# Performance work log

Hardware: AMD Instinct MI355X
Metric: run time of the kernel (lower is better)

## Reference

```python
import jax, jax.numpy as jnp
import numpy as np


def setup_inputs() -> dict:
    key = jax.random.key(0)
    k1, k2, k3 = jax.random.split(key, 3)
    bs, seqlen, hidden = 2, 2048, 1024
    s, h = 4, 256  # sqrt_n_heads, head_size
    std = 0.02
    num_layers = 12
    hidden_states = jax.random.normal(k1, (bs, seqlen, hidden), dtype=jnp.float32)
    q_scale = 1.0 / np.sqrt(2.0 * num_layers * h)
    queries = jax.random.normal(k2, (s, h, h * s), dtype=jnp.float32) * std * q_scale
    combiners = jax.random.normal(k3, (s, h * s, h), dtype=jnp.float32) * (std * q_scale)
    return {"hidden_states": hidden_states, "queries": queries, "combiners": combiners}


def reference(hidden_states, queries, combiners):
    # queries: [s1, h, s*h], combiners: [s1, s*h, h]
    s, h, _ = queries.shape
    bs, S, E = hidden_states.shape
    x = hidden_states.reshape(bs, S, s, h)            # [b, t, s, h]
    qw = queries.reshape(s, h, s, h)                  # [s1, h_in, s2, h_out]
    # projected queries, already permuted to [s2, b, t, s1, f]
    Q = jnp.einsum('btae,aeqf->qbtaf', x, qw)
    # pre-attention scores: [s2, b, t, s1, u] (u = key position)  ~O(S^2)
    pre = jnp.einsum('qbtaf,buqf->qbtau', Q, x)
    # attention output, permuted to [s1, b, t, s2, g]
    attn = jnp.einsum('qbtau,buqg->abtqg', pre, x)
    attn = attn.reshape(s, bs, S, s * h)              # [s1, b, t, s2*h]
    out = jnp.einsum('abtk,akg->btag', attn, combiners)
    return out.reshape(bs, S, s * h)
```

## Files before the change

kernel.cpp:

```cpp
#include <hip/hip_runtime.h>
#include <hip/hip_bf16.h>


typedef unsigned short u16;
using short8  = __attribute__((ext_vector_type(8))) short;
using floatx4 = __attribute__((ext_vector_type(4))) float;

__device__ inline u16 f2bf(float f) {
    unsigned u = __float_as_uint(f);
    unsigned r = u + 0x7fffu + ((u >> 16) & 1u);
    return (u16)(r >> 16);
}

template <typename T>
__device__ inline void stage64(const T* __restrict__ src, long ld,
                               u16* __restrict__ dst, int tid) {
#pragma unroll
    for (int it = 0; it < 4; ++it) {
        const int flat = (it * 256 + tid) * 4;
        const int kl = flat & 63, rl = flat >> 6;
        ushort4 v;
        if (sizeof(T) == 4) {
            const float4 f = *(const float4*)&((const float*)src)[(long)rl * ld + kl];
            v.x = f2bf(f.x); v.y = f2bf(f.y); v.z = f2bf(f.z); v.w = f2bf(f.w);
        } else {
            v = *(const ushort4*)&((const u16*)src)[(long)rl * ld + kl];
        }
        const int chunk = ((kl >> 5) * 4 + (rl >> 4)) * 64 + ((kl >> 3) & 3) * 16 + (rl & 15);
        *(ushort4*)&dst[chunk * 8 + (kl & 7)] = v;
    }
}

__device__ inline void stage64_sum8(const float* __restrict__ s0, long ld,
                                    long partStride,
                                    u16* __restrict__ dst, int tid) {
#pragma unroll
    for (int it = 0; it < 4; ++it) {
        const int flat = (it * 256 + tid) * 4;
        const int kl = flat & 63, rl = flat >> 6;
        const long off = (long)rl * ld + kl;
        float4 acc = *(const float4*)&s0[off];
#pragma unroll
        for (int s = 1; s < 8; ++s) {
            const float4 f = *(const float4*)&s0[(long)s * partStride + off];
            acc.x += f.x; acc.y += f.y; acc.z += f.z; acc.w += f.w;
        }
        ushort4 v;
        v.x = f2bf(acc.x); v.y = f2bf(acc.y); v.z = f2bf(acc.z); v.w = f2bf(acc.w);
        const int chunk = ((kl >> 5) * 4 + (rl >> 4)) * 64 + ((kl >> 3) & 3) * 16 + (rl & 15);
        *(ushort4*)&dst[chunk * 8 + (kl & 7)] = v;
    }
}

__device__ inline void stage_km64(const float* __restrict__ src, long ld,
                                  u16* __restrict__ dst, int tid) {
#pragma unroll
    for (int it = 0; it < 4; ++it) {
        const int flat = (it * 256 + tid) * 4;
        const int m = flat & 63, k = flat >> 6;
        const float4 f = *(const float4*)&src[(long)k * ld + m];
        const int cb_ = ((k >> 5) * 4 + (m >> 4)) * 64 + ((k & 31) >> 3) * 16 + (m & 15);
        const int j = k & 7;
        dst[(cb_ + 0) * 8 + j] = f2bf(f.x);
        dst[(cb_ + 1) * 8 + j] = f2bf(f.y);
        dst[(cb_ + 2) * 8 + j] = f2bf(f.z);
        dst[(cb_ + 3) * 8 + j] = f2bf(f.w);
    }
}

template <typename TA, typename TB, typename TC,
          bool AKM, bool BKM, bool BSUM8, bool ATOMIC>
__device__ inline void gemm_tile(const TA* __restrict__ A, long lda,
                                 const TB* __restrict__ B, long ldb,
                                 long partStride,
                                 TC* __restrict__ C, long ldc,
                                 int m0, int n0) {
    __shared__ u16 As[16384];
    __shared__ u16 Bs[16384];
    const int tid = threadIdx.x, lane = tid & 63, w = tid >> 6;
    const int IA = (w & 1) * 2, JB = (w >> 1) * 2;
    floatx4 acc[2][2] = {};

#pragma unroll
    for (int kb = 0; kb < 4; ++kb) {
        if (AKM) stage_km64((const float*)A + (long)(kb * 64) * lda, lda, As + kb * 4096, tid);
        else     stage64(A + kb * 64, lda, As + kb * 4096, tid);
    }
#pragma unroll
    for (int kb = 0; kb < 4; ++kb) {
        if (BSUM8)    stage64_sum8((const float*)B + kb * 64, ldb, partStride, Bs + kb * 4096, tid);
        else if (BKM) stage_km64((const float*)B + (long)(kb * 64) * ldb, ldb, Bs + kb * 4096, tid);
        else          stage64(B + kb * 64, ldb, Bs + kb * 4096, tid);
    }
    __syncthreads();

#pragma unroll
    for (int kb = 0; kb < 4; ++kb)
#pragma unroll
        for (int s = 0; s < 2; ++s) {
            short8 af[2], bfr[2];
#pragma unroll
            for (int i = 0; i < 2; ++i)
                af[i] = *(const short8*)&As[kb * 4096 + ((s * 4 + IA + i) * 64 + lane) * 8];
#pragma unroll
            for (int j = 0; j < 2; ++j)
                bfr[j] = *(const short8*)&Bs[kb * 4096 + ((s * 4 + JB + j) * 64 + lane) * 8];
#pragma unroll
            for (int i = 0; i < 2; ++i)
#pragma unroll
                for (int j = 0; j < 2; ++j)
                    acc[i][j] = __builtin_amdgcn_mfma_f32_16x16x32_bf16(af[i], bfr[j], acc[i][j], 0, 0, 0);
        }

    const int rb = (lane >> 4) * 4, col = lane & 15;
#pragma unroll
    for (int i = 0; i < 2; ++i)
#pragma unroll
        for (int j = 0; j < 2; ++j)
#pragma unroll
            for (int r = 0; r < 4; ++r) {
                const int gm = m0 + (IA + i) * 16 + rb + r;
                const int gn = n0 + (JB + j) * 16 + col;
                TC* p = &C[(long)gm * ldc + gn];
                if (sizeof(TC) == 2) *(u16*)p = f2bf(acc[i][j][r]);
                else if (ATOMIC) atomicAdd((float*)p, acc[i][j][r]);
                else *(float*)p = acc[i][j][r];
            }
}

__global__ __launch_bounds__(256) void k_cvt(const float* __restrict__ x,
                                             u16* __restrict__ xbf) {
    const long i = ((long)blockIdx.x * 256 + threadIdx.x) * 8;
    const float4 a = *(const float4*)&x[i];
    const float4 b = *(const float4*)&x[i + 4];
    ushort4 lo, hi;
    lo.x = f2bf(a.x); lo.y = f2bf(a.y); lo.z = f2bf(a.z); lo.w = f2bf(a.w);
    hi.x = f2bf(b.x); hi.y = f2bf(b.y); hi.z = f2bf(b.z); hi.w = f2bf(b.w);
    *(ushort4*)&xbf[i]     = lo;
    *(ushort4*)&xbf[i + 4] = hi;
}

__global__ __launch_bounds__(256) void k_gred(const float* __restrict__ Gp,
                                              float* __restrict__ Gs) {
    const long i = ((long)blockIdx.x * 256 + threadIdx.x) * 4;
    float4 acc = *(const float4*)&Gp[i];
#pragma unroll
    for (int s = 1; s < 8; ++s) {
        const float4 f = *(const float4*)&Gp[(long)s * 524288 + i];
        acc.x += f.x; acc.y += f.y; acc.z += f.z; acc.w += f.w;
    }
    *(float4*)&Gs[i] = acc;
}

__device__ inline void stage_km128_bf(const u16* __restrict__ src, long ld,
                                      u16* __restrict__ dst, int tid) {
#pragma unroll
    for (int it = 0; it < 4; ++it) {
        const int flat = (it * 256 + tid) * 8;
        const int m = flat & 127, k = flat >> 7;
        const short8 v = *(const short8*)&src[(long)k * ld + m];
        const int cb_ = ((k >> 5) * 8 + (m >> 4)) * 64 + ((k & 31) >> 3) * 16 + (m & 15);
        const int j = k & 7;
#pragma unroll
        for (int e = 0; e < 8; ++e)
            dst[(cb_ + e) * 8 + j] = (u16)v[e];
    }
}

__global__ __launch_bounds__(256) void k_gram(const u16* __restrict__ xbf,
                                              float* __restrict__ Gp,
                                              float* __restrict__ Wt) {
    __shared__ u16 As[16384];
    __shared__ u16 Bs[16384];
    const int tl = blockIdx.x, bq = blockIdx.y, split = blockIdx.z;
    const int tm = tl >> 1, tn = tl & 1;
    const int b = bq >> 2, q = bq & 3;
    const int tid = threadIdx.x, lane = tid & 63, w = tid >> 6;
    const int IA2 = (w & 1), JB2 = (w >> 1);

    {
        const int bl = tl + 4 * bq + 32 * split;
        float4 zero = {0.f, 0.f, 0.f, 0.f};
        float4* wz = (float4*)(Wt + (long)bl * 2048) + tid;
        wz[0] = zero; wz[256] = zero;
    }

    const u16* base = xbf + (long)b * 2097152 + (long)split * 256 * 1024 + q * 256;
    const u16* A = base + tm * 128;
    const u16* B = base + tn * 128;
    floatx4 acc[4][4] = {};

#pragma unroll
    for (int burst = 0; burst < 2; ++burst) {
        if (burst) __syncthreads();
#pragma unroll
        for (int kb = 0; kb < 2; ++kb) {
            const long kk = burst * 128 + kb * 64;
            stage_km128_bf(A + kk * 1024, 1024, As + kb * 8192, tid);
            stage_km128_bf(B + kk * 1024, 1024, Bs + kb * 8192, tid);
        }
        __syncthreads();
#pragma unroll
        for (int kb = 0; kb < 2; ++kb)
#pragma unroll
            for (int s = 0; s < 2; ++s) {
                short8 af[4], bfr[4];
#pragma unroll
                for (int i = 0; i < 4; ++i)
                    af[i] = *(const short8*)&As[kb * 8192 + ((s * 8 + IA2 * 4 + i) * 64 + lane) * 8];
#pragma unroll
                for (int j = 0; j < 4; ++j)
                    bfr[j] = *(const short8*)&Bs[kb * 8192 + ((s * 8 + JB2 * 4 + j) * 64 + lane) * 8];
#pragma unroll
                for (int i = 0; i < 4; ++i)
#pragma unroll
                    for (int j = 0; j < 4; ++j)
                        acc[i][j] = __builtin_amdgcn_mfma_f32_16x16x32_bf16(af[i], bfr[j], acc[i][j], 0, 0, 0);
            }
    }

    float* C = Gp + (long)(split * 8 + bq) * 65536;
    const int rb = (lane >> 4) * 4, col = lane & 15;
#pragma unroll
    for (int i = 0; i < 4; ++i)
#pragma unroll
        for (int j = 0; j < 4; ++j)
#pragma unroll
            for (int r = 0; r < 4; ++r) {
                const int gm = tm * 128 + IA2 * 64 + i * 16 + rb + r;
                const int gn = tn * 128 + JB2 * 64 + j * 16 + col;
                C[(long)gm * 256 + gn] = acc[i][j][r];
            }
}

__global__ __launch_bounds__(256) void k_2a(const float* __restrict__ comb,
                                            const float* __restrict__ Gs,
                                            u16* __restrict__ Tt) {
    const int tile = blockIdx.x, i = blockIdx.y;
    const int tm = tile >> 2, tn = tile & 3;
    const int q = i & 3, ba = i >> 2, b = ba >> 2, a = ba & 3;
    gemm_tile<float, float, u16, true, false, false, false>(
        comb + (long)a * 262144 + (long)q * 256 * 256 + tm * 64, 256,
        Gs + (long)(b * 4 + q) * 65536 + (long)tn * 64 * 256, 256,
        0,
        Tt + (long)ba * 262144, 1024,
        tm * 64, q * 256 + tn * 64);
}

__global__ __launch_bounds__(256) void k_2b(const u16* __restrict__ Tt,
                                            const float* __restrict__ qw,
                                            float* __restrict__ Wt) {
    const int tile = blockIdx.x, ba = blockIdx.y, split = blockIdx.z;
    const int tm = tile >> 2, tn = tile & 3;
    const int a = ba & 3;
    gemm_tile<u16, float, float, false, false, false, true>(
        Tt + (long)ba * 262144 + (long)tm * 64 * 1024 + split * 256, 1024,
        qw + (long)a * 262144 + (long)tn * 64 * 1024 + split * 256, 1024, 0,
        Wt + (long)ba * 65536, 256,
        tm * 64, tn * 64);
}

__global__ __launch_bounds__(256) void k_3(const u16* __restrict__ xbf,
                                           const float* __restrict__ Wt,
                                           float* __restrict__ out) {
    const int tl = blockIdx.x, ba = blockIdx.y;
    const int tm = tl >> 2, tn = tl & 3;
    const int b = ba >> 2, a = ba & 3;
    gemm_tile<u16, float, float, false, false, false, false>(
        xbf + (long)b * 2097152 + (long)tm * 64 * 1024 + a * 256, 1024,
        Wt + (long)ba * 65536 + (long)tn * 64 * 256, 256, 0,
        out + (long)b * 2097152 + a * 256, 1024,
        tm * 64, tn * 64);
}

extern "C" void kernel_launch(void* const* d_in, const int* in_sizes, int n_in,
                              void* d_out, int out_size, void* d_ws, size_t ws_size,
                              hipStream_t stream) {
    const float* x    = (const float*)d_in[0];
    const float* qw   = (const float*)d_in[1];
    const float* comb = (const float*)d_in[2];
    float* out = (float*)d_out;

    char* ws = (char*)d_ws;
    float* Gp = (float*)(ws);
    float* Wt = (float*)(ws + (16u << 20));
    u16*   Tt = (u16*)  (ws + (18u << 20));
    float* Gs = (float*)(ws + (22u << 20));
    u16*   xbf= (u16*)  (ws + (24u << 20));

    k_cvt <<<dim3(2048),     256, 0, stream>>>(x, xbf);
    k_gram<<<dim3(4, 8, 8),  256, 0, stream>>>(xbf, Gp, Wt);
    k_gred<<<dim3(512),      256, 0, stream>>>(Gp, Gs);
    k_2a  <<<dim3(16, 32),   256, 0, stream>>>(comb, Gs, Tt);
    k_2b  <<<dim3(16, 8, 4), 256, 0, stream>>>(Tt, qw, Wt);
    k_3   <<<dim3(128, 8),   256, 0, stream>>>(xbf, Wt, out);
}
```

Before: 133.7 us.

## Pre-convert weights to bf16, drop atomics in k_2b, store intermediates as bf16

A single prep kernel now converts x, queries, and a transposed combiners tensor to bf16 up front. All GEMM stages then stage only bf16 operands with 16-byte loads. k_2b loops over the full K with four rounds instead of a 4-way split with atomicAdd, which also removes the Wt zeroing. Gs and Wt are stored as bf16, halving their traffic. The cost is an extra transpose pass, fewer blocks in k_2b (128 instead of 512), and slightly more rounding in the intermediates.

```diff
diff --git a/kernel.cpp b/kernel.cpp
--- a/kernel.cpp
+++ b/kernel.cpp
@@ -12,69 +12,23 @@
     return (u16)(r >> 16);
 }
 
-template <typename T>
-__device__ inline void stage64(const T* __restrict__ src, long ld,
-                               u16* __restrict__ dst, int tid) {
-#pragma unroll
-    for (int it = 0; it < 4; ++it) {
-        const int flat = (it * 256 + tid) * 4;
+__device__ inline void stage64_bf(const u16* __restrict__ src, long ld,
+                                  u16* __restrict__ dst, int tid) {
+#pragma unroll
+    for (int it = 0; it < 2; ++it) {
+        const int flat = (it * 256 + tid) * 8;
         const int kl = flat & 63, rl = flat >> 6;
-        ushort4 v;
-        if (sizeof(T) == 4) {
-            const float4 f = *(const float4*)&((const float*)src)[(long)rl * ld + kl];
-            v.x = f2bf(f.x); v.y = f2bf(f.y); v.z = f2bf(f.z); v.w = f2bf(f.w);
-        } else {
-            v = *(const ushort4*)&((const u16*)src)[(long)rl * ld + kl];
-        }
+        const short8 v = *(const short8*)&src[(long)rl * ld + kl];
         const int chunk = ((kl >> 5) * 4 + (rl >> 4)) * 64 + ((kl >> 3) & 3) * 16 + (rl & 15);
-        *(ushort4*)&dst[chunk * 8 + (kl & 7)] = v;
-    }
-}
-
-__device__ inline void stage64_sum8(const float* __restrict__ s0, long ld,
-                                    long partStride,
-                                    u16* __restrict__ dst, int tid) {
-#pragma unroll
-    for (int it = 0; it < 4; ++it) {
-        const int flat = (it * 256 + tid) * 4;
-        const int kl = flat & 63, rl = flat >> 6;
-        const long off = (long)rl * ld + kl;
-        float4 acc = *(const float4*)&s0[off];
-#pragma unroll
-        for (int s = 1; s < 8; ++s) {
-            const float4 f = *(const float4*)&s0[(long)s * partStride + off];
-            acc.x += f.x; acc.y += f.y; acc.z += f.z; acc.w += f.w;
-        }
-        ushort4 v;
-        v.x = f2bf(acc.x); v.y = f2bf(acc.y); v.z = f2bf(acc.z); v.w = f2bf(acc.w);
-        const int chunk = ((kl >> 5) * 4 + (rl >> 4)) * 64 + ((kl >> 3) & 3) * 16 + (rl & 15);
-        *(ushort4*)&dst[chunk * 8 + (kl & 7)] = v;
-    }
-}
-
-__device__ inline void stage_km64(const float* __restrict__ src, long ld,
-                                  u16* __restrict__ dst, int tid) {
-#pragma unroll
-    for (int it = 0; it < 4; ++it) {
-        const int flat = (it * 256 + tid) * 4;
-        const int m = flat & 63, k = flat >> 6;
-        const float4 f = *(const float4*)&src[(long)k * ld + m];
-        const int cb_ = ((k >> 5) * 4 + (m >> 4)) * 64 + ((k & 31) >> 3) * 16 + (m & 15);
-        const int j = k & 7;
-        dst[(cb_ + 0) * 8 + j] = f2bf(f.x);
-        dst[(cb_ + 1) * 8 + j] = f2bf(f.y);
-        dst[(cb_ + 2) * 8 + j] = f2bf(f.z);
-        dst[(cb_ + 3) * 8 + j] = f2bf(f.w);
-    }
-}
-
-template <typename TA, typename TB, typename TC,
-          bool AKM, bool BKM, bool BSUM8, bool ATOMIC>
-__device__ inline void gemm_tile(const TA* __restrict__ A, long lda,
-                                 const TB* __restrict__ B, long ldb,
-                                 long partStride,
-                                 TC* __restrict__ C, long ldc,
-                                 int m0, int n0) {
+        *(short8*)&dst[chunk * 8] = v;
+    }
+}
+
+template <typename TC, int KR>
+__device__ inline void gemm64(const u16* __restrict__ A, long lda,
+                              const u16* __restrict__ B, long ldb,
+                              TC* __restrict__ C, long ldc,
+                              int m0, int n0) {
     __shared__ u16 As[16384];
     __shared__ u16 Bs[16384];
     const int tid = threadIdx.x, lane = tid & 63, w = tid >> 6;
@@ -82,35 +36,35 @@
     floatx4 acc[2][2] = {};
 
 #pragma unroll
-    for (int kb = 0; kb < 4; ++kb) {
-        if (AKM) stage_km64((const float*)A + (long)(kb * 64) * lda, lda, As + kb * 4096, tid);
-        else     stage64(A + kb * 64, lda, As + kb * 4096, tid);
-    }
-#pragma unroll
-    for (int kb = 0; kb < 4; ++kb) {
-        if (BSUM8)    stage64_sum8((const float*)B + kb * 64, ldb, partStride, Bs + kb * 4096, tid);
-        else if (BKM) stage_km64((const float*)B + (long)(kb * 64) * ldb, ldb, Bs + kb * 4096, tid);
-        else          stage64(B + kb * 64, ldb, Bs + kb * 4096, tid);
-    }
-    __syncthreads();
-
-#pragma unroll
-    for (int kb = 0; kb < 4; ++kb)
-#pragma unroll
-        for (int s = 0; s < 2; ++s) {
-            short8 af[2], bfr[2];
-#pragma unroll
-            for (int i = 0; i < 2; ++i)
-                af[i] = *(const short8*)&As[kb * 4096 + ((s * 4 + IA + i) * 64 + lane) * 8];
-#pragma unroll
-            for (int j = 0; j < 2; ++j)
-                bfr[j] = *(const short8*)&Bs[kb * 4096 + ((s * 4 + JB + j) * 64 + lane) * 8];
-#pragma unroll
-            for (int i = 0; i < 2; ++i)
+    for (int r = 0; r < KR; ++r) {
+        if (r) __syncthreads();
+        const u16* Ar = A + r * 256;
+        const u16* Br = B + r * 256;
+#pragma unroll
+        for (int kb = 0; kb < 4; ++kb) {
+            stage64_bf(Ar + kb * 64, lda, As + kb * 4096, tid);
+            stage64_bf(Br + kb * 64, ldb, Bs + kb * 4096, tid);
+        }
+        __syncthreads();
+
+#pragma unroll
+        for (int kb = 0; kb < 4; ++kb)
+#pragma unroll
+            for (int s = 0; s < 2; ++s) {
+                short8 af[2], bfr[2];
+#pragma unroll
+                for (int i = 0; i < 2; ++i)
+                    af[i] = *(const short8*)&As[kb * 4096 + ((s * 4 + IA + i) * 64 + lane) * 8];
 #pragma unroll
                 for (int j = 0; j < 2; ++j)
-                    acc[i][j] = __builtin_amdgcn_mfma_f32_16x16x32_bf16(af[i], bfr[j], acc[i][j], 0, 0, 0);
-        }
+                    bfr[j] = *(const short8*)&Bs[kb * 4096 + ((s * 4 + JB + j) * 64 + lane) * 8];
+#pragma unroll
+                for (int i = 0; i < 2; ++i)
+#pragma unroll
+                    for (int j = 0; j < 2; ++j)
+                        acc[i][j] = __builtin_amdgcn_mfma_f32_16x16x32_bf16(af[i], bfr[j], acc[i][j], 0, 0, 0);
+            }
+    }
 
     const int rb = (lane >> 4) * 4, col = lane & 15;
 #pragma unroll
@@ -123,25 +77,57 @@
                 const int gn = n0 + (JB + j) * 16 + col;
                 TC* p = &C[(long)gm * ldc + gn];
                 if (sizeof(TC) == 2) *(u16*)p = f2bf(acc[i][j][r]);
-                else if (ATOMIC) atomicAdd((float*)p, acc[i][j][r]);
-                else *(float*)p = acc[i][j][r];
-            }
-}
-
-__global__ __launch_bounds__(256) void k_cvt(const float* __restrict__ x,
-                                             u16* __restrict__ xbf) {
-    const long i = ((long)blockIdx.x * 256 + threadIdx.x) * 8;
-    const float4 a = *(const float4*)&x[i];
-    const float4 b = *(const float4*)&x[i + 4];
-    ushort4 lo, hi;
-    lo.x = f2bf(a.x); lo.y = f2bf(a.y); lo.z = f2bf(a.z); lo.w = f2bf(a.w);
-    hi.x = f2bf(b.x); hi.y = f2bf(b.y); hi.z = f2bf(b.z); hi.w = f2bf(b.w);
-    *(ushort4*)&xbf[i]     = lo;
-    *(ushort4*)&xbf[i + 4] = hi;
+                else                 *(float*)p = acc[i][j][r];
+            }
+}
+
+__global__ __launch_bounds__(256) void k_prep(const float* __restrict__ x,
+                                              const float* __restrict__ qw,
+                                              const float* __restrict__ comb,
+                                              u16* __restrict__ xbf,
+                                              u16* __restrict__ qwbf,
+                                              u16* __restrict__ combt) {
+    const int bx = blockIdx.x, tid = threadIdx.x;
+    __shared__ u16 T[64][66];
+    if (bx < 2560) {
+        const float* src = bx < 2048 ? x : qw;
+        u16* dst = bx < 2048 ? xbf : qwbf;
+        const long i = ((long)(bx < 2048 ? bx : bx - 2048) * 256 + tid) * 8;
+        const float4 a = *(const float4*)&src[i];
+        const float4 b = *(const float4*)&src[i + 4];
+        ushort4 lo, hi;
+        lo.x = f2bf(a.x); lo.y = f2bf(a.y); lo.z = f2bf(a.z); lo.w = f2bf(a.w);
+        hi.x = f2bf(b.x); hi.y = f2bf(b.y); hi.z = f2bf(b.z); hi.w = f2bf(b.w);
+        *(ushort4*)&dst[i]     = lo;
+        *(ushort4*)&dst[i + 4] = hi;
+    } else {
+        const int t = bx - 2560;
+        const int a = t >> 6;
+        const int qh0 = ((t >> 2) & 15) * 64, g0 = (t & 3) * 64;
+        const float* src = comb + (long)a * 262144;
+        u16* dst = combt + (long)a * 262144;
+#pragma unroll
+        for (int it = 0; it < 4; ++it) {
+            const int flat = (it * 256 + tid) * 4;
+            const int r = flat >> 6, c = flat & 63;
+            const float4 f = *(const float4*)&src[(long)(qh0 + r) * 256 + g0 + c];
+            T[r][c]     = f2bf(f.x); T[r][c + 1] = f2bf(f.y);
+            T[r][c + 2] = f2bf(f.z); T[r][c + 3] = f2bf(f.w);
+        }
+        __syncthreads();
+#pragma unroll
+        for (int it = 0; it < 4; ++it) {
+            const int flat = (it * 256 + tid) * 4;
+            const int r = flat >> 6, c = flat & 63;
+            ushort4 v;
+            v.x = T[c][r]; v.y = T[c + 1][r]; v.z = T[c + 2][r]; v.w = T[c + 3][r];
+            *(ushort4*)&dst[(long)(g0 + r) * 1024 + qh0 + c] = v;
+        }
+    }
 }
 
 __global__ __launch_bounds__(256) void k_gred(const float* __restrict__ Gp,
-                                              float* __restrict__ Gs) {
+                                              u16* __restrict__ Gs) {
     const long i = ((long)blockIdx.x * 256 + threadIdx.x) * 4;
     float4 acc = *(const float4*)&Gp[i];
 #pragma unroll
@@ -149,7 +135,9 @@
         const float4 f = *(const float4*)&Gp[(long)s * 524288 + i];
         acc.x += f.x; acc.y += f.y; acc.z += f.z; acc.w += f.w;
     }
-    *(float4*)&Gs[i] = acc;
+    ushort4 v;
+    v.x = f2bf(acc.x); v.y = f2bf(acc.y); v.z = f2bf(acc.z); v.w = f2bf(acc.w);
+    *(ushort4*)&Gs[i] = v;
 }
 
 __device__ inline void stage_km128_bf(const u16* __restrict__ src, long ld,
@@ -168,8 +156,7 @@
 }
 
 __global__ __launch_bounds__(256) void k_gram(const u16* __restrict__ xbf,
-                                              float* __restrict__ Gp,
-                                              float* __restrict__ Wt) {
+                                              float* __restrict__ Gp) {
     __shared__ u16 As[16384];
     __shared__ u16 Bs[16384];
     const int tl = blockIdx.x, bq = blockIdx.y, split = blockIdx.z;
@@ -178,13 +165,6 @@
     const int tid = threadIdx.x, lane = tid & 63, w = tid >> 6;
     const int IA2 = (w & 1), JB2 = (w >> 1);
 
-    {
-        const int bl = tl + 4 * bq + 32 * split;
-        float4 zero = {0.f, 0.f, 0.f, 0.f};
-        float4* wz = (float4*)(Wt + (long)bl * 2048) + tid;
-        wz[0] = zero; wz[256] = zero;
-    }
-
     const u16* base = xbf + (long)b * 2097152 + (long)split * 256 * 1024 + q * 256;
     const u16* A = base + tm * 128;
     const u16* B = base + tn * 128;
@@ -233,42 +213,41 @@
             }
 }
 
-__global__ __launch_bounds__(256) void k_2a(const float* __restrict__ comb,
-                                            const float* __restrict__ Gs,
+__global__ __launch_bounds__(256) void k_2a(const u16* __restrict__ combt,
+                                            const u16* __restrict__ Gs,
                                             u16* __restrict__ Tt) {
     const int tile = blockIdx.x, i = blockIdx.y;
     const int tm = tile >> 2, tn = tile & 3;
     const int q = i & 3, ba = i >> 2, b = ba >> 2, a = ba & 3;
-    gemm_tile<float, float, u16, true, false, false, false>(
-        comb + (long)a * 262144 + (long)q * 256 * 256 + tm * 64, 256,
+    gemm64<u16, 1>(
+        combt + (long)a * 262144 + (long)tm * 64 * 1024 + q * 256, 1024,
         Gs + (long)(b * 4 + q) * 65536 + (long)tn * 64 * 256, 256,
-        0,
         Tt + (long)ba * 262144, 1024,
         tm * 64, q * 256 + tn * 64);
 }
 
 __global__ __launch_bounds__(256) void k_2b(const u16* __restrict__ Tt,
-                                            const float* __restrict__ qw,
-                                            float* __restrict__ Wt) {
-    const int tile = blockIdx.x, ba = blockIdx.y, split = blockIdx.z;
+                                            const u16* __restrict__ qwbf,
+                                            u16* __restrict__ Wt) {
+    const int tile = blockIdx.x, ba = blockIdx.y;
     const int tm = tile >> 2, tn = tile & 3;
     const int a = ba & 3;
-    gemm_tile<u16, float, float, false, false, false, true>(
-        Tt + (long)ba * 262144 + (long)tm * 64 * 1024 + split * 256, 1024,
-        qw + (long)a * 262144 + (long)tn * 64 * 1024 + split * 256, 1024, 0,
+    gemm64<u16, 4>(
+        Tt + (long)ba * 262144 + (long)tm * 64 * 1024, 1024,
+        qwbf + (long)a * 262144 + (long)tn * 64 * 1024, 1024,
         Wt + (long)ba * 65536, 256,
         tm * 64, tn * 64);
 }
 
 __global__ __launch_bounds__(256) void k_3(const u16* __restrict__ xbf,
-                                           const float* __restrict__ Wt,
+                                           const u16* __restrict__ Wt,
                                            float* __restrict__ out) {
     const int tl = blockIdx.x, ba = blockIdx.y;
     const int tm = tl >> 2, tn = tl & 3;
     const int b = ba >> 2, a = ba & 3;
-    gemm_tile<u16, float, float, false, false, false, false>(
+    gemm64<float, 1>(
         xbf + (long)b * 2097152 + (long)tm * 64 * 1024 + a * 256, 1024,
-        Wt + (long)ba * 65536 + (long)tn * 64 * 256, 256, 0,
+        Wt + (long)ba * 65536 + (long)tn * 64 * 256, 256,
         out + (long)b * 2097152 + a * 256, 1024,
         tm * 64, tn * 64);
 }
@@ -282,16 +261,18 @@
     float* out = (float*)d_out;
 
     char* ws = (char*)d_ws;
-    float* Gp = (float*)(ws);
-    float* Wt = (float*)(ws + (16u << 20));
-    u16*   Tt = (u16*)  (ws + (18u << 20));
-    float* Gs = (float*)(ws + (22u << 20));
-    u16*   xbf= (u16*)  (ws + (24u << 20));
-
-    k_cvt <<<dim3(2048),     256, 0, stream>>>(x, xbf);
-    k_gram<<<dim3(4, 8, 8),  256, 0, stream>>>(xbf, Gp, Wt);
-    k_gred<<<dim3(512),      256, 0, stream>>>(Gp, Gs);
-    k_2a  <<<dim3(16, 32),   256, 0, stream>>>(comb, Gs, Tt);
-    k_2b  <<<dim3(16, 8, 4), 256, 0, stream>>>(Tt, qw, Wt);
-    k_3   <<<dim3(128, 8),   256, 0, stream>>>(xbf, Wt, out);
-}
+    float* Gp   = (float*)(ws);
+    u16*   xbf  = (u16*)  (ws + (16u << 20));
+    u16*   Tt   = (u16*)  (ws + (24u << 20));
+    u16*   qwbf = (u16*)  (ws + (28u << 20));
+    u16*   combt= (u16*)  (ws + (30u << 20));
+    u16*   Gsbf = (u16*)  (ws + (32u << 20));
+    u16*   Wtbf = (u16*)  (ws + (33u << 20));
+
+    k_prep<<<dim3(2816),    256, 0, stream>>>(x, qw, comb, xbf, qwbf, combt);
+    k_gram<<<dim3(4, 8, 8), 256, 0, stream>>>(xbf, Gp);
+    k_gred<<<dim3(512),     256, 0, stream>>>(Gp, Gsbf);
+    k_2a  <<<dim3(16, 32),  256, 0, stream>>>(combt, Gsbf, Tt);
+    k_2b  <<<dim3(16, 8),   256, 0, stream>>>(Tt, qwbf, Wtbf);
+    k_3   <<<dim3(128, 8),  256, 0, stream>>>(xbf, Wtbf, out);
+}
```

New measurement: 132.1 us. No clear change (-1.2%).
